# Kernel tuning notes

Measured on AMD Instinct MI355X. Metric: run time of the kernel, lower is better.

The kernel has to match this reference:

```python
import jax, jax.numpy as jnp
import numpy as np

DIM = 512
HEADS = 8
WIN = 64
HIDDEN = 2048
EPS = 1e-5


def layernorm(x, g, b):
    mu = jnp.mean(x, axis=-1, keepdims=True)
    var = jnp.var(x, axis=-1, keepdims=True)
    return (x - mu) * jax.lax.rsqrt(var + EPS) * g + b


def setup_inputs() -> dict:
    key = jax.random.key(0)
    ks = jax.random.split(key, 10)
    s = lambda fan_in: 1.0 / np.sqrt(fan_in)
    return {
        "x": jax.random.normal(ks[0], (8, 4096, DIM), dtype=jnp.float32),
        "ln1_g": jnp.ones((DIM,), jnp.float32),
        "ln1_b": jnp.zeros((DIM,), jnp.float32),
        "qkv_w": jax.random.normal(ks[1], (DIM, 3 * DIM), jnp.float32) * s(DIM),
        "qkv_b": jnp.zeros((3 * DIM,), jnp.float32),
        "proj_w": jax.random.normal(ks[2], (DIM, DIM), jnp.float32) * s(DIM),
        "proj_b": jnp.zeros((DIM,), jnp.float32),
        "ln2_g": jnp.ones((DIM,), jnp.float32),
        "ln2_b": jnp.zeros((DIM,), jnp.float32),
        "fc1_w": jax.random.normal(ks[3], (DIM, HIDDEN), jnp.float32) * s(DIM),
        "fc1_b": jnp.zeros((HIDDEN,), jnp.float32),
        "fc2_w": jax.random.normal(ks[4], (HIDDEN, DIM), jnp.float32) * s(HIDDEN),
        "fc2_b": jnp.zeros((DIM,), jnp.float32),
    }


def reference(x, ln1_g, ln1_b, qkv_w, qkv_b, proj_w, proj_b, ln2_g, ln2_b,
              fc1_w, fc1_b, fc2_w, fc2_b):
    B, N, C = x.shape
    hd = C // HEADS
    scale = hd ** -0.5

    # --- W-MSA (shift_size forced to 0, attn_mask None) ---
    h = layernorm(x, ln1_g, ln1_b)
    hw = h.reshape(B * (N // WIN), WIN, C)
    qkv = hw @ qkv_w + qkv_b
    qkv = qkv.reshape(-1, WIN, 3, HEADS, hd)
    q = qkv[:, :, 0] * scale
    k = qkv[:, :, 1]
    v = qkv[:, :, 2]
    attn = jnp.einsum('bqhd,bkhd->bhqk', q, k)
    attn = jax.nn.softmax(attn, axis=-1)
    o = jnp.einsum('bhqk,bkhd->bqhd', attn, v).reshape(-1, WIN, C)
    o = o @ proj_w + proj_b
    x = x + o.reshape(B, N, C)

    # --- MLP (GELU exact, dropout=0) ---
    h2 = layernorm(x, ln2_g, ln2_b)
    h2 = jax.nn.gelu(h2 @ fc1_w + fc1_b, approximate=False)
    x = x + (h2 @ fc2_w + fc2_b)
    return x
```

## Files before the change

kernel.cpp:

```cpp
#include <hip/hip_runtime.h>
#include <hip/hip_bf16.h>
#include <cstdint>

typedef unsigned short U16;
typedef float f32x4 __attribute__((ext_vector_type(4)));
typedef __bf16 bf16x8 __attribute__((ext_vector_type(8)));

#define DEVINL __device__ __forceinline__

DEVINL U16 f2bf(float f) {
    unsigned u = __float_as_uint(f);
    return (U16)((u + 0x7FFFu + ((u >> 16) & 1u)) >> 16);
}
DEVINL float bf2f(U16 s) { return __uint_as_float(((unsigned)s) << 16); }

DEVINL void gld16(const void* g, void* l) {
    __builtin_amdgcn_global_load_lds(
        (const __attribute__((address_space(1))) void*)g,
        (__attribute__((address_space(3))) void*)l, 16, 0, 0);
}

#define MFMA_BF16 __builtin_amdgcn_mfma_f32_16x16x32_bf16

__global__ __launch_bounds__(256) void tcast_kernel(const float* __restrict__ w,
                                                    U16* __restrict__ wt, int K, int N) {
    __shared__ float tile[32][33];
    int n0 = blockIdx.x * 32, k0 = blockIdx.y * 32;
    int tx = threadIdx.x, ty = threadIdx.y;
#pragma unroll
    for (int i = 0; i < 32; i += 8) tile[ty + i][tx] = w[(size_t)(k0 + ty + i) * N + (n0 + tx)];
    __syncthreads();
#pragma unroll
    for (int i = 0; i < 32; i += 8) wt[(size_t)(n0 + ty + i) * K + (k0 + tx)] = f2bf(tile[tx][ty + i]);
}

__global__ __launch_bounds__(256) void ln_kernel(const float* __restrict__ x,
                                                 const float* __restrict__ g,
                                                 const float* __restrict__ b,
                                                 U16* __restrict__ out) {
    int lane = threadIdx.x & 63;
    size_t row = (size_t)blockIdx.x * 4 + (threadIdx.x >> 6);
    const float4* xr = (const float4*)(x + row * 512);
    float4 v0 = xr[lane], v1 = xr[lane + 64];
    float s = (v0.x + v0.y) + (v0.z + v0.w) + (v1.x + v1.y) + (v1.z + v1.w);
    float sq = (v0.x * v0.x + v0.y * v0.y + v0.z * v0.z + v0.w * v0.w) +
               (v1.x * v1.x + v1.y * v1.y + v1.z * v1.z + v1.w * v1.w);
#pragma unroll
    for (int m = 1; m < 64; m <<= 1) { s += __shfl_xor(s, m); sq += __shfl_xor(sq, m); }
    float mu = s * (1.f / 512.f);
    float var = sq * (1.f / 512.f) - mu * mu;
    float rs = rsqrtf(var + 1e-5f);
    const float4* g4 = (const float4*)g;
    const float4* b4 = (const float4*)b;
    float4 gv = g4[lane], bv = b4[lane];
    ushort4 o;
    o.x = f2bf((v0.x - mu) * rs * gv.x + bv.x);
    o.y = f2bf((v0.y - mu) * rs * gv.y + bv.y);
    o.z = f2bf((v0.z - mu) * rs * gv.z + bv.z);
    o.w = f2bf((v0.w - mu) * rs * gv.w + bv.w);
    ((ushort4*)(out + row * 512))[lane] = o;
    gv = g4[lane + 64]; bv = b4[lane + 64];
    o.x = f2bf((v1.x - mu) * rs * gv.x + bv.x);
    o.y = f2bf((v1.y - mu) * rs * gv.y + bv.y);
    o.z = f2bf((v1.z - mu) * rs * gv.z + bv.z);
    o.w = f2bf((v1.w - mu) * rs * gv.w + bv.w);
    ((ushort4*)(out + row * 512))[lane + 64] = o;
}

template <int EPI, int K>
__global__ __launch_bounds__(256, 3) void gemm_rt(const U16* __restrict__ A,
                                                  const U16* __restrict__ Bt,
                                                  const float* __restrict__ bias,
                                                  const float* __restrict__ resid,
                                                  U16* __restrict__ outb,
                                                  float* __restrict__ outf,
                                                  int M, int N, int gridN) {
    __shared__ __align__(16) U16 smem[16384];

    const int tid = threadIdx.x;
    const int lane = tid & 63, wv = tid >> 6;
    const int lo = lane & 15, hi = lane >> 4;
    const int wm = wv >> 1, wn = wv & 1;

    const int nwg = gridDim.x, bid = blockIdx.x;
    const int swzb = (bid & 7) * (nwg >> 3) + (bid >> 3);
    const int bn = swzb % gridN, bm = swzb / gridN;

    const int sr = tid >> 2;
    const int lc = (tid & 3) ^ ((sr >> 1) & 3);
    const U16* gA0 = A + (size_t)(bm * 128 + sr) * K + lc * 8;
    const U16* gA1 = gA0 + (size_t)64 * K;
    const U16* gB0 = Bt + (size_t)(bn * 128 + sr) * K + lc * 8;
    const U16* gB1 = gB0 + (size_t)64 * K;

    const int ck = (hi ^ ((lo >> 1) & 3)) << 3;
    const int aoff = (wm * 64 + lo) * 32 + ck;
    const int boff = 4096 + (wn * 64 + lo) * 32 + ck;

    f32x4 acc[4][4] = {};
    bf16x8 afA[4], bgA[4], afB[4], bgB[4];

#define RD(AF, BG, CB)                                                          \
    do {                                                                        \
        const U16* _Ab = smem + (CB) + aoff;                                    \
        const U16* _Bb = smem + (CB) + boff;                                    \
        _Pragma("unroll") for (int i = 0; i < 4; ++i)                           \
            AF[i] = *(const bf16x8*)(_Ab + i * 512);                            \
        _Pragma("unroll") for (int j = 0; j < 4; ++j)                           \
            BG[j] = *(const bf16x8*)(_Bb + j * 512);                            \
    } while (0)

#define MM(AF, BG)                                                              \
    do {                                                                        \
        __builtin_amdgcn_s_setprio(1);                                          \
        _Pragma("unroll") for (int i = 0; i < 4; ++i)                           \
            _Pragma("unroll") for (int j = 0; j < 4; ++j)                       \
                acc[i][j] = MFMA_BF16(AF[i], BG[j], acc[i][j], 0, 0, 0);        \
        __builtin_amdgcn_s_setprio(0);                                          \
    } while (0)

#define ITER(tt, TREL, LIM)                                                     \
    do {                                                                        \
        if ((TREL) + 2 < (LIM)) {                                               \
            U16* _l = smem + (((tt)&1) ? 8192 : 0) + tid * 8;                   \
            gld16(gAc0 + ((tt) + 2) * 32, _l);                                  \
            gld16(gAc1 + ((tt) + 2) * 32, _l + 2048);                           \
            gld16(gBc0 + ((tt) + 2) * 32, _l + 4096);                           \
            gld16(gBc1 + ((tt) + 2) * 32, _l + 6144);                           \
            asm volatile("s_waitcnt vmcnt(4)" ::: "memory");                    \
        } else {                                                                \
            asm volatile("s_waitcnt vmcnt(0)" ::: "memory");                    \
        }                                                                       \
        __builtin_amdgcn_s_barrier();                                           \
        if ((TREL) + 1 < (LIM)) {                                               \
            const int _cb = (((tt) + 1) & 1) ? 8192 : 0;                        \
            if (((tt)&1) == 0) RD(afB, bgB, _cb); else RD(afA, bgA, _cb);       \
        }                                                                       \
        __builtin_amdgcn_sched_barrier(0x8);                                    \
        if (((tt)&1) == 0) MM(afA, bgA); else MM(afB, bgB);                     \
        asm volatile("s_waitcnt lgkmcnt(0)" ::: "memory");                      \
        __builtin_amdgcn_s_barrier();                                           \
    } while (0)

    constexpr int NT = K >> 5;
    static_assert(NT >= 16 && (NT % 16) == 0, "K must be a multiple of 512");

    {
        U16* _l = smem + tid * 8;
        gld16(gA0, _l);          gld16(gA1, _l + 2048);
        gld16(gB0, _l + 4096);   gld16(gB1, _l + 6144);
        U16* _l2 = smem + 8192 + tid * 8;
        gld16(gA0 + 32, _l2);        gld16(gA1 + 32, _l2 + 2048);
        gld16(gB0 + 32, _l2 + 4096); gld16(gB1 + 32, _l2 + 6144);
    }
    asm volatile("s_waitcnt vmcnt(4)" ::: "memory");
    __builtin_amdgcn_s_barrier();
    RD(afA, bgA, 0);

    for (int t0 = 0; t0 + 16 < NT; t0 += 16) {
        const U16* gAc0 = gA0 + (size_t)t0 * 32;
        const U16* gAc1 = gA1 + (size_t)t0 * 32;
        const U16* gBc0 = gB0 + (size_t)t0 * 32;
        const U16* gBc1 = gB1 + (size_t)t0 * 32;
#pragma unroll
        for (int tt = 0; tt < 16; ++tt) ITER(tt, tt, 1 << 30);
    }
    {
        constexpr int t0 = NT - 16;
        const U16* gAc0 = gA0 + (size_t)t0 * 32;
        const U16* gAc1 = gA1 + (size_t)t0 * 32;
        const U16* gBc0 = gB0 + (size_t)t0 * 32;
        const U16* gBc1 = gB1 + (size_t)t0 * 32;
#pragma unroll
        for (int tt = 0; tt < 16; ++tt) ITER(tt, tt, 16);
    }

    const int row0 = bm * 128 + wm * 64 + hi * 4;
    const int col0 = bn * 128 + wn * 64 + lo;
    float bc[4];
#pragma unroll
    for (int j = 0; j < 4; ++j) bc[j] = bias[col0 + j * 16];

    if (EPI == 1) {
#pragma unroll
        for (int i = 0; i < 4; ++i)
#pragma unroll
            for (int r = 0; r < 4; ++r) {
                const size_t rowb = (size_t)(row0 + i * 16 + r) * N;
#pragma unroll
                for (int j = 0; j < 4; ++j) {
                    const size_t idx = rowb + col0 + j * 16;
                    outf[idx] = acc[i][j][r] + bc[j] + resid[idx];
                }
            }
    } else {
#pragma unroll
        for (int i = 0; i < 4; ++i)
#pragma unroll
            for (int j = 0; j < 4; ++j)
#pragma unroll
                for (int r = 0; r < 4; ++r) {
                    float v = acc[i][j][r] + bc[j];
                    if (EPI == 2) {
                        float u = v * (0.7978845608028654f + 0.0356774081f * v * v);
                        v = v / (1.f + __expf(-2.f * u));
                    }
                    outb[(size_t)(row0 + i * 16 + r) * N + col0 + j * 16] = f2bf(v);
                }
    }
#undef ITER
#undef MM
#undef RD
}

__global__ __launch_bounds__(256) void attn_kernel(const U16* __restrict__ qkv,
                                                   U16* __restrict__ o) {
    const int blk = blockIdx.x;
    const int w = blk >> 3, h = blk & 7;
    const int tid = threadIdx.x;
    const int lane = tid & 63, wv = tid >> 6;
    const int lo = lane & 15, hi = lane >> 4;

    __shared__ __align__(16) U16 Qs[64][72];
    __shared__ __align__(16) U16 Ks[64][72];
    __shared__ __align__(16) U16 Vt[64][72];
    __shared__ __align__(16) U16 Ps[4][16][72];

    {
        const int r = tid >> 2;
        const int c0 = (tid & 3) << 4;
        const U16* p = qkv + (size_t)(w * 64 + r) * 1536 + h * 64 + c0;
        *(bf16x8*)&Ks[r][c0] = *(const bf16x8*)(p + 512);
        *(bf16x8*)&Ks[r][c0 + 8] = *(const bf16x8*)(p + 520);
        const U16* pv = p + 1024;
#pragma unroll
        for (int i = 0; i < 16; i++) Vt[c0 + i][r] = pv[i];
#pragma unroll
        for (int i = 0; i < 16; i++) Qs[r][c0 + i] = f2bf(bf2f(p[i]) * 0.125f);
    }
    __syncthreads();

    const int rb = wv * 16;
    f32x4 s[4] = {};
#pragma unroll
    for (int dc = 0; dc < 64; dc += 32) {
        bf16x8 a = *(const bf16x8*)&Qs[rb + lo][dc + hi * 8];
#pragma unroll
        for (int jb = 0; jb < 4; jb++) {
            bf16x8 bfr = *(const bf16x8*)&Ks[jb * 16 + lo][dc + hi * 8];
            s[jb] = MFMA_BF16(a, bfr, s[jb], 0, 0, 0);
        }
    }
#pragma unroll
    for (int r = 0; r < 4; r++) {
        float m = fmaxf(fmaxf(s[0][r], s[1][r]), fmaxf(s[2][r], s[3][r]));
#pragma unroll
        for (int msk = 1; msk < 16; msk <<= 1) m = fmaxf(m, __shfl_xor(m, msk));
        float e[4], sum = 0.f;
#pragma unroll
        for (int jb = 0; jb < 4; jb++) { e[jb] = expf(s[jb][r] - m); sum += e[jb]; }
#pragma unroll
        for (int msk = 1; msk < 16; msk <<= 1) sum += __shfl_xor(sum, msk);
        float inv = 1.f / sum;
#pragma unroll
        for (int jb = 0; jb < 4; jb++) Ps[wv][hi * 4 + r][jb * 16 + lo] = f2bf(e[jb] * inv);
    }
    __syncthreads();

    f32x4 oa[4] = {};
#pragma unroll
    for (int jc = 0; jc < 64; jc += 32) {
        bf16x8 a = *(const bf16x8*)&Ps[wv][lo][jc + hi * 8];
#pragma unroll
        for (int db = 0; db < 4; db++) {
            bf16x8 bfr = *(const bf16x8*)&Vt[db * 16 + lo][jc + hi * 8];
            oa[db] = MFMA_BF16(a, bfr, oa[db], 0, 0, 0);
        }
    }
#pragma unroll
    for (int db = 0; db < 4; db++)
#pragma unroll
        for (int r = 0; r < 4; r++)
            o[(size_t)(w * 64 + rb + hi * 4 + r) * 512 + h * 64 + db * 16 + lo] = f2bf(oa[db][r]);
}

extern "C" void kernel_launch(void* const* d_in, const int* in_sizes, int n_in,
                              void* d_out, int out_size, void* d_ws, size_t ws_size,
                              hipStream_t stream) {
    const float* x = (const float*)d_in[0];
    const float* ln1_g = (const float*)d_in[1];
    const float* ln1_b = (const float*)d_in[2];
    const float* qkv_w = (const float*)d_in[3];
    const float* qkv_b = (const float*)d_in[4];
    const float* proj_w = (const float*)d_in[5];
    const float* proj_b = (const float*)d_in[6];
    const float* ln2_g = (const float*)d_in[7];
    const float* ln2_b = (const float*)d_in[8];
    const float* fc1_w = (const float*)d_in[9];
    const float* fc1_b = (const float*)d_in[10];
    const float* fc2_w = (const float*)d_in[11];
    const float* fc2_b = (const float*)d_in[12];
    float* out = (float*)d_out;

    char* ws = (char*)d_ws;
    U16* hbuf = (U16*)ws;
    U16* big = (U16*)(ws + 33554432);
    U16* wt_qkv = (U16*)(ws + 33554432 + 134217728);
    U16* wt_proj = wt_qkv + 1536 * 512;
    U16* wt_fc1 = wt_proj + 512 * 512;
    U16* wt_fc2 = wt_fc1 + 2048 * 512;

    dim3 tb(32, 8);
    tcast_kernel<<<dim3(1536 / 32, 512 / 32), tb, 0, stream>>>(qkv_w, wt_qkv, 512, 1536);
    tcast_kernel<<<dim3(512 / 32, 512 / 32), tb, 0, stream>>>(proj_w, wt_proj, 512, 512);
    tcast_kernel<<<dim3(2048 / 32, 512 / 32), tb, 0, stream>>>(fc1_w, wt_fc1, 512, 2048);
    tcast_kernel<<<dim3(512 / 32, 2048 / 32), tb, 0, stream>>>(fc2_w, wt_fc2, 2048, 512);

    ln_kernel<<<8192, 256, 0, stream>>>(x, ln1_g, ln1_b, hbuf);
    gemm_rt<0, 512><<<3072, 256, 0, stream>>>(hbuf, wt_qkv, qkv_b, nullptr, big, nullptr, 32768, 1536, 12);
    attn_kernel<<<4096, 256, 0, stream>>>(big, hbuf);
    gemm_rt<1, 512><<<1024, 256, 0, stream>>>(hbuf, wt_proj, proj_b, x, nullptr, out, 32768, 512, 4);
    ln_kernel<<<8192, 256, 0, stream>>>(out, ln2_g, ln2_b, hbuf);
    gemm_rt<2, 512><<<4096, 256, 0, stream>>>(hbuf, wt_fc1, fc1_b, nullptr, big, nullptr, 32768, 2048, 16);
    gemm_rt<1, 2048><<<1024, 256, 0, stream>>>(big, wt_fc2, fc2_b, out, nullptr, out, 32768, 512, 4);
}
```

Before: 377.5 us.

## Load B fragments directly from global into registers, staging only A in LDS

The GEMM now streams only the A tile through LDS, double-buffered at half the previous shared memory. B fragments are read straight from global memory into registers one k-step ahead. This is meant to cut LDS traffic and footprint, which may allow more resident workgroups. In exchange, each wave redundantly loads B from global/L2 (two waves share each B column slice), B loads use narrow strided accesses, and the prefetch depth drops from two stages to one.

```diff
diff --git a/kernel.cpp b/kernel.cpp
--- a/kernel.cpp
+++ b/kernel.cpp
@@ -75,7 +75,7 @@
                                                   U16* __restrict__ outb,
                                                   float* __restrict__ outf,
                                                   int M, int N, int gridN) {
-    __shared__ __align__(16) U16 smem[16384];
+    __shared__ __align__(16) U16 smem[8192];
 
     const int tid = threadIdx.x;
     const int lane = tid & 63, wv = tid >> 6;
@@ -90,55 +90,50 @@
     const int lc = (tid & 3) ^ ((sr >> 1) & 3);
     const U16* gA0 = A + (size_t)(bm * 128 + sr) * K + lc * 8;
     const U16* gA1 = gA0 + (size_t)64 * K;
-    const U16* gB0 = Bt + (size_t)(bn * 128 + sr) * K + lc * 8;
-    const U16* gB1 = gB0 + (size_t)64 * K;
+
+    const U16* gBf = Bt + (size_t)(bn * 128 + wn * 64 + lo) * K + hi * 8;
 
     const int ck = (hi ^ ((lo >> 1) & 3)) << 3;
     const int aoff = (wm * 64 + lo) * 32 + ck;
-    const int boff = 4096 + (wn * 64 + lo) * 32 + ck;
 
     f32x4 acc[4][4] = {};
-    bf16x8 afA[4], bgA[4], afB[4], bgB[4];
-
-#define RD(AF, BG, CB)                                                          \
+    bf16x8 af[4], bgA[4], bgB[4];
+
+#define LOADB(BG, kof)                                                          \
     do {                                                                        \
-        const U16* _Ab = smem + (CB) + aoff;                                    \
-        const U16* _Bb = smem + (CB) + boff;                                    \
-        _Pragma("unroll") for (int i = 0; i < 4; ++i)                           \
-            AF[i] = *(const bf16x8*)(_Ab + i * 512);                            \
         _Pragma("unroll") for (int j = 0; j < 4; ++j)                           \
-            BG[j] = *(const bf16x8*)(_Bb + j * 512);                            \
+            BG[j] = *(const bf16x8*)(gBc + (size_t)j * 16 * K + (kof));         \
     } while (0)
 
-#define MM(AF, BG)                                                              \
+#define MM(BG)                                                                  \
     do {                                                                        \
         __builtin_amdgcn_s_setprio(1);                                          \
         _Pragma("unroll") for (int i = 0; i < 4; ++i)                           \
             _Pragma("unroll") for (int j = 0; j < 4; ++j)                       \
-                acc[i][j] = MFMA_BF16(AF[i], BG[j], acc[i][j], 0, 0, 0);        \
+                acc[i][j] = MFMA_BF16(af[i], BG[j], acc[i][j], 0, 0, 0);        \
         __builtin_amdgcn_s_setprio(0);                                          \
     } while (0)
 
-#define ITER(tt, TREL, LIM)                                                     \
+#define ITER(tt, LIM)                                                           \
     do {                                                                        \
-        if ((TREL) + 2 < (LIM)) {                                               \
-            U16* _l = smem + (((tt)&1) ? 8192 : 0) + tid * 8;                   \
-            gld16(gAc0 + ((tt) + 2) * 32, _l);                                  \
-            gld16(gAc1 + ((tt) + 2) * 32, _l + 2048);                           \
-            gld16(gBc0 + ((tt) + 2) * 32, _l + 4096);                           \
-            gld16(gBc1 + ((tt) + 2) * 32, _l + 6144);                           \
-            asm volatile("s_waitcnt vmcnt(4)" ::: "memory");                    \
+        if ((tt) + 1 < (LIM)) {                                                 \
+            U16* _l = smem + ((((tt) + 1) & 1) ? 4096 : 0) + tid * 8;           \
+            gld16(gAc0 + ((tt) + 1) * 32, _l);                                  \
+            gld16(gAc1 + ((tt) + 1) * 32, _l + 2048);                           \
+            if (((tt) & 1) == 0) LOADB(bgB, ((tt) + 1) * 32);                   \
+            else                 LOADB(bgA, ((tt) + 1) * 32);                   \
+            asm volatile("s_waitcnt vmcnt(6)" ::: "memory");                    \
         } else {                                                                \
             asm volatile("s_waitcnt vmcnt(0)" ::: "memory");                    \
         }                                                                       \
         __builtin_amdgcn_s_barrier();                                           \
-        if ((TREL) + 1 < (LIM)) {                                               \
-            const int _cb = (((tt) + 1) & 1) ? 8192 : 0;                        \
-            if (((tt)&1) == 0) RD(afB, bgB, _cb); else RD(afA, bgA, _cb);       \
+        {                                                                       \
+            const U16* _Ab = smem + (((tt) & 1) ? 4096 : 0) + aoff;             \
+            _Pragma("unroll") for (int i = 0; i < 4; ++i)                       \
+                af[i] = *(const bf16x8*)(_Ab + i * 512);                        \
         }                                                                       \
-        __builtin_amdgcn_sched_barrier(0x8);                                    \
-        if (((tt)&1) == 0) MM(afA, bgA); else MM(afB, bgB);                     \
-        asm volatile("s_waitcnt lgkmcnt(0)" ::: "memory");                      \
+        if (((tt) & 1) == 0) MM(bgA);                                           \
+        else                 MM(bgB);                                           \
         __builtin_amdgcn_s_barrier();                                           \
     } while (0)
 
@@ -147,32 +142,26 @@
 
     {
         U16* _l = smem + tid * 8;
-        gld16(gA0, _l);          gld16(gA1, _l + 2048);
-        gld16(gB0, _l + 4096);   gld16(gB1, _l + 6144);
-        U16* _l2 = smem + 8192 + tid * 8;
-        gld16(gA0 + 32, _l2);        gld16(gA1 + 32, _l2 + 2048);
-        gld16(gB0 + 32, _l2 + 4096); gld16(gB1 + 32, _l2 + 6144);
-    }
-    asm volatile("s_waitcnt vmcnt(4)" ::: "memory");
-    __builtin_amdgcn_s_barrier();
-    RD(afA, bgA, 0);
+        gld16(gA0, _l);
+        gld16(gA1, _l + 2048);
+        const U16* gBc = gBf;
+        LOADB(bgA, 0);
+    }
 
     for (int t0 = 0; t0 + 16 < NT; t0 += 16) {
         const U16* gAc0 = gA0 + (size_t)t0 * 32;
         const U16* gAc1 = gA1 + (size_t)t0 * 32;
-        const U16* gBc0 = gB0 + (size_t)t0 * 32;
-        const U16* gBc1 = gB1 + (size_t)t0 * 32;
-#pragma unroll
-        for (int tt = 0; tt < 16; ++tt) ITER(tt, tt, 1 << 30);
+        const U16* gBc = gBf + (size_t)t0 * 32;
+#pragma unroll
+        for (int tt = 0; tt < 16; ++tt) ITER(tt, 1 << 30);
     }
     {
         constexpr int t0 = NT - 16;
         const U16* gAc0 = gA0 + (size_t)t0 * 32;
         const U16* gAc1 = gA1 + (size_t)t0 * 32;
-        const U16* gBc0 = gB0 + (size_t)t0 * 32;
-        const U16* gBc1 = gB1 + (size_t)t0 * 32;
-#pragma unroll
-        for (int tt = 0; tt < 16; ++tt) ITER(tt, tt, 16);
+        const U16* gBc = gBf + (size_t)t0 * 32;
+#pragma unroll
+        for (int tt = 0; tt < 16; ++tt) ITER(tt, 16);
     }
 
     const int row0 = bm * 128 + wm * 64 + hi * 4;
@@ -210,7 +199,7 @@
     }
 #undef ITER
 #undef MM
-#undef RD
+#undef LOADB
 }
 
 __global__ __launch_bounds__(256) void attn_kernel(const U16* __restrict__ qkv,
```

New measurement: 535.9 us. 42.0% more time.
